# Kernel tuning notes

Measured on AMD Instinct MI355X. Metric: run time of the kernel, lower is better.

The kernel has to match this reference:

```python
import jax, jax.numpy as jnp
import numpy as np

JITTER = 1e-6
ND = 20       # num_draws
STEPS = 10    # num_steps
G = 100       # num_gammas: PG truncation terms
NUM_CLASSES = 2


def _rbf(X, outputscale, lengthscale):
    x2 = jnp.sum(X * X, axis=-1)
    d2 = jnp.maximum(x2[:, None] + x2[None, :] - 2.0 * (X @ X.T), 0.0)
    return outputscale * jnp.exp(-0.5 * d2 / (lengthscale * lengthscale))


def _chol(K):
    return jnp.linalg.cholesky(K + JITTER * jnp.eye(K.shape[-1], dtype=K.dtype))


def _pg_draw(key, c):
    # PG(1, c) via truncated infinite gamma convolution (G terms):
    # omega = (1/(2 pi^2)) * sum_k Exp(1) / ((k-1/2)^2 + c^2/(4 pi^2))
    ks = jnp.arange(1, G + 1, dtype=c.dtype)
    denom = (ks - 0.5) ** 2 + (c[..., None] ** 2) / (4.0 * jnp.pi ** 2)
    e = jax.random.exponential(key, c.shape + (G,), dtype=c.dtype)
    return jnp.sum(e / denom, axis=-1) / (2.0 * jnp.pi ** 2)


def reference(X, Y, outputscale, lengthscale):
    N = X.shape[0]
    os_ = outputscale[0]
    ls = lengthscale[0]
    K = _rbf(X, os_, ls)                          # [N,N]
    Kinv = jnp.linalg.inv(K + JITTER * jnp.eye(N, dtype=X.dtype))
    L = _chol(K)
    mu = jnp.zeros((N,), X.dtype)                 # zero mean GP
    Kinv_mu = Kinv @ mu
    y_oh = 1.0 - jax.nn.one_hot(Y, NUM_CLASSES, dtype=X.dtype)
    kappa = y_oh[:, 0] - 0.5                      # binary => 1 stick, N_sb = 1

    key = jax.random.key(42)
    k_init, k_om0, k_loop = jax.random.split(key, 3)

    # initial Gibbs state: f ~ N(mu, K) per draw
    eps0 = jax.random.normal(k_init, (ND, N), X.dtype)
    f = mu[None, :] + jnp.einsum('ij,dj->di', L, eps0)
    omega = jax.lax.stop_gradient(_pg_draw(k_om0, jax.lax.stop_gradient(f)))

    def body(state, kk):
        omega_c, f_c = state
        k1, k2 = jax.random.split(kk)
        A = Kinv[None] + jax.vmap(jnp.diag)(omega_c)         # [ND,N,N]
        sigma = jnp.linalg.inv(A)
        mu_t = jnp.einsum('dij,j->di', sigma, kappa + Kinv_mu)
        Lt = _chol(sigma)
        eps = jax.random.normal(k1, (ND, N), X.dtype)
        f_new = mu_t + jnp.einsum('dij,dj->di', Lt, eps)
        omega_new = jax.lax.stop_gradient(_pg_draw(k2, jax.lax.stop_gradient(f_new)))
        return (omega_new, f_new), None

    (omega, f), _ = jax.lax.scan(body, (omega, f), jax.random.split(k_loop, STEPS))

    # marginal log likelihood given omega (PG draws are constants)
    om = jnp.clip(omega, 1e-16)                  # [ND,N]
    Sigma_z = K[None] + jax.vmap(jnp.diag)(1.0 / om)
    Lz = _chol(Sigma_z)
    z = kappa[None, :] / om
    diff = z - mu[None, :]
    sol = jax.scipy.linalg.solve_triangular(Lz, diff[..., None], lower=True)[..., 0]
    quad = jnp.sum(sol * sol, axis=-1)
    logdet = jnp.sum(jnp.log(jnp.diagonal(Lz, axis1=-2, axis2=-1)), axis=-1)
    log2pi = float(np.log(2.0 * np.pi))
    logp = -0.5 * quad - logdet - 0.5 * N * log2pi
    mll = (logp + 0.5 * N * log2pi
           - 0.5 * jnp.sum(jnp.log(om), axis=-1)
           + 0.5 * jnp.sum(kappa[None, :] ** 2 / om, axis=-1)
           - N * float(np.log(2.0)))
    nmll = -jnp.mean(mll)
    return nmll / N


def setup_inputs() -> dict:
    key = jax.random.key(0)
    kx, ky, ko, kl = jax.random.split(key, 4)
    X = jax.random.normal(kx, (1024, 64), jnp.float32)
    Y = jax.random.randint(ky, (1024,), 0, 2)
    outputscale = jax.random.uniform(ko, (1,), jnp.float32) + 0.5
    # rescale lengthscale to ~sqrt(d) so exp(-d2/2ls^2) doesn't underflow
    lengthscale = (jax.random.uniform(kl, (1,), jnp.float32) + 0.5) * 8.0
    return {"X": X, "Y": Y, "outputscale": outputscale, "lengthscale": lengthscale}
```

## Files before the change

### kernel.cpp

```cpp
#include <hip/hip_runtime.h>
#include <stdint.h>

#define NPTS 1024
#define NDRAWS 20
#define NSTEPS 10
#define NG 100
#define PARTITIONABLE 1

#define TRI(i) (((i) * ((i) + 1)) / 2)
#define NTILE 16
#define NTRI 136
#define AST ((size_t)NTRI * 4096)

typedef unsigned int u32;

__host__ __device__ static inline void tf2x32(u32 k0, u32 k1, u32 x0, u32 x1, u32* o0, u32* o1){
  u32 ks2 = k0 ^ k1 ^ 0x1BD11BDAu;
  x0 += k0; x1 += k1;
#define TFR(r) { x0 += x1; x1 = (x1 << r) | (x1 >> (32 - r)); x1 ^= x0; }
  TFR(13) TFR(15) TFR(26) TFR(6)
  x0 += k1; x1 += ks2 + 1u;
  TFR(17) TFR(29) TFR(16) TFR(24)
  x0 += ks2; x1 += k0 + 2u;
  TFR(13) TFR(15) TFR(26) TFR(6)
  x0 += k0; x1 += k1 + 3u;
  TFR(17) TFR(29) TFR(16) TFR(24)
  x0 += k1; x1 += ks2 + 4u;
  TFR(13) TFR(15) TFR(26) TFR(6)
  x0 += ks2; x1 += k0 + 5u;
#undef TFR
  *o0 = x0; *o1 = x1;
}

__device__ static inline u32 rand32(u32 ka, u32 kb, u32 i, u32 total){
  u32 a, b;
#if PARTITIONABLE
  (void)total;
  tf2x32(ka, kb, 0u, i, &a, &b);
  return a ^ b;
#else
  u32 h = total >> 1;
  if (i < h){ tf2x32(ka, kb, i, i + h, &a, &b); return a; }
  else      { tf2x32(ka, kb, i - h, i, &a, &b); return b; }
#endif
}

__device__ static inline float u01f(u32 bits){
  return __uint_as_float(0x3F800000u | (bits >> 9)) - 1.0f;
}

__device__ static inline float erfinv32(float x){
  float w = -log1pf(-x * x);
  float p;
  if (w < 5.0f){
    w -= 2.5f;
    p = 2.81022636e-08f;
    p = fmaf(p, w, 3.43273939e-07f);
    p = fmaf(p, w, -3.5233877e-06f);
    p = fmaf(p, w, -4.39150654e-06f);
    p = fmaf(p, w, 0.00021858087f);
    p = fmaf(p, w, -0.00125372503f);
    p = fmaf(p, w, -0.00417768164f);
    p = fmaf(p, w, 0.246640727f);
    p = fmaf(p, w, 1.50140941f);
  } else {
    w = sqrtf(w) - 3.0f;
    p = -0.000200214257f;
    p = fmaf(p, w, 0.000100950558f);
    p = fmaf(p, w, 0.00134934322f);
    p = fmaf(p, w, -0.00367342844f);
    p = fmaf(p, w, 0.00573950773f);
    p = fmaf(p, w, -0.0076224613f);
    p = fmaf(p, w, 0.00943887047f);
    p = fmaf(p, w, 1.00167406f);
    p = fmaf(p, w, 2.83297682f);
  }
  return p * x;
}

__device__ static inline float normal_from_bits(u32 bits){
  const float LO = -0.99999994f;
  float u = u01f(bits);
  float v = u * 2.0f + LO;
  v = fmaxf(LO, v);
  return 1.4142135623730951f * erfinv32(v);
}

__device__ inline float  tsqrt(float x){ return sqrtf(x); }
__device__ inline double tsqrt(double x){ return sqrt(x); }
__device__ inline float  tmax(float a, float b){ return fmaxf(a, b); }
__device__ inline double tmax(double a, double b){ return fmax(a, b); }

__device__ inline void tri_decode(int p, int& ti, int& tj){
  int t = (int)((sqrtf(8.0f * (float)p + 1.0f) - 1.0f) * 0.5f);
  while ((t + 1) * (t + 2) / 2 <= p) ++t;
  while (t * (t + 1) / 2 > p) --t;
  ti = t; tj = p - t * (t + 1) / 2;
}

__device__ inline void chol_inv_64(float (*t)[65], float (*Xs)[65], float* diagL, int tid){
  for (int idx = tid; idx < 4096; idx += 256){
    int r = idx >> 6, c = idx & 63;
    Xs[r][c] = (r == c) ? 1.0f : 0.0f;
  }
  __syncthreads();
  for (int j = 0; j < 64; ++j){
    float piv = sqrtf(fmaxf(t[j][j], 1e-30f));
    float inv = 1.0f / piv;
    if (tid < 64){
      int r = j + 1 + tid;
      if (r < 64) t[r][j] *= inv;
      if (tid == 0) diagL[j] = piv;
    } else if (tid < 128){
      Xs[j][tid - 64] *= inv;
    }
    __syncthreads();
    int tg = tid >> 6, tr = tid & 63;
    for (int r2 = j + 1 + tg; r2 < 64; r2 += 4){
      float lj = t[r2][j];
      int c = j + 1 + tr;
      if (c <= r2) t[r2][c] -= lj * t[c][j];
      Xs[r2][tr] = fmaf(-lj, Xs[j][tr], Xs[r2][tr]);
    }
    __syncthreads();
  }
  if (tid < 64) t[tid][tid] = diagL[tid];
  __syncthreads();
}

__global__ __launch_bounds__(256) void k_prep(const float* X, const int* Y, float* x2, float* kappaf){
  int n = blockIdx.x * 256 + threadIdx.x;
  if (n >= NPTS) return;
  float s = 0.f;
  for (int d = 0; d < 64; ++d){ float v = X[n * 64 + d]; s += v * v; }
  x2[n] = s;
  kappaf[NPTS - 1 - n] = (float)Y[n] - 0.5f;
}

__global__ void k_computeK(const float* X, const float* x2, const float* osp, const float* lsp,
                           double* Ld){
  int j = blockIdx.x * 16 + threadIdx.x;
  int i = blockIdx.y * 16 + threadIdx.y;
  float os = osp[0], ls = lsp[0];
  float dot = 0.f;
  for (int d = 0; d < 64; ++d) dot += X[i * 64 + d] * X[j * 64 + d];
  float d2 = x2[i] + x2[j] - 2.0f * dot;
  d2 = fmaxf(d2, 0.0f);
  float kv = os * expf((-0.5f * d2) / (ls * ls));
  Ld[(size_t)i * NPTS + j] = (double)kv + (i == j ? 1e-6 : 0.0);
}

__global__ __launch_bounds__(256) void k_castL(const double* Ld, float* Lf){
  int idx = blockIdx.x * 256 + threadIdx.x;
  int i = idx >> 10, j = idx & 1023;
  Lf[idx] = (j <= i) ? (float)Ld[idx] : 0.0f;
}

__global__ __launch_bounds__(256) void k_logdetK(const double* Ld, float* ldetK){
  __shared__ double red[4];
  int tid = threadIdx.x;
  double s = 0.0;
  for (int i = tid; i < NPTS; i += 256) s += log(Ld[(size_t)i * NPTS + i]);
  for (int o = 32; o; o >>= 1) s += __shfl_down(s, o);
  if ((tid & 63) == 0) red[tid >> 6] = s;
  __syncthreads();
  if (tid == 0) ldetK[0] = (float)(2.0 * (red[0] + red[1] + red[2] + red[3]));
}

__global__ __launch_bounds__(256) void k_chol_diag_inv_d(double* M, double* Dinv, int p){
  double* DI = Dinv + (size_t)p * 4096;
  int k0 = p * 64;
  __shared__ double t[64][65];
  __shared__ double Xs[64][65];
  int tid = threadIdx.x;
  for (int idx = tid; idx < 4096; idx += 256){
    int r = idx >> 6, c = idx & 63;
    t[r][c] = (c <= r) ? M[(size_t)(k0 + r) * NPTS + k0 + c] : 0.0;
    Xs[r][c] = (r == c) ? 1.0 : 0.0;
  }
  __syncthreads();
  for (int j = 0; j < 64; ++j){
    double piv = tsqrt(tmax(t[j][j], 1e-300));
    double inv = 1.0 / piv;
    __syncthreads();
    if (tid == 0) t[j][j] = piv;
    for (int r = j + 1 + tid; r < 64; r += 256) t[r][j] *= inv;
    __syncthreads();
    int tr = tid & 63, tg = tid >> 6;
    for (int r = j + 1 + tg; r < 64; r += 4){
      int c = j + 1 + tr;
      if (c <= r) t[r][c] -= t[r][j] * t[c][j];
    }
    __syncthreads();
  }
  for (int idx = tid; idx < 4096; idx += 256){
    int r = idx >> 6, c = idx & 63;
    M[(size_t)(k0 + r) * NPTS + k0 + c] = (c <= r) ? t[r][c] : 0.0;
  }
  if (tid < 64){
    int c = tid;
    Xs[c][c] = 1.0 / t[c][c];
    for (int r = c + 1; r < 64; ++r){
      double s = 0.0;
      for (int k = c; k < r; ++k) s += t[r][k] * Xs[k][c];
      Xs[r][c] = -s / t[r][r];
    }
    for (int r = 0; r < c; ++r) Xs[r][c] = 0.0;
  }
  __syncthreads();
  for (int idx = tid; idx < 4096; idx += 256){
    int r = idx >> 6, c = idx & 63;
    DI[idx] = Xs[r][c];
  }
}

__global__ __launch_bounds__(256) void k_chol_panel_d(double* M, const double* Dinv, int p){
  const double* DI = Dinv + (size_t)p * 4096;
  int r0 = (p + 1) * 64 + blockIdx.x * 64;
  __shared__ double Rs[64][65];
  __shared__ double Ds[64][65];
  int tid = threadIdx.x;
  for (int idx = tid; idx < 4096; idx += 256){
    int r = idx >> 6, c = idx & 63;
    Rs[r][c] = M[(size_t)(r0 + r) * NPTS + p * 64 + c];
    Ds[r][c] = DI[idx];
  }
  __syncthreads();
  int tx = tid & 15, ty = tid >> 4;
  double acc[4][4];
#pragma unroll
  for (int a = 0; a < 4; ++a)
#pragma unroll
    for (int b = 0; b < 4; ++b) acc[a][b] = 0.0;
  for (int k = 0; k < 64; ++k){
    double av[4], bv[4];
#pragma unroll
    for (int a = 0; a < 4; ++a) av[a] = Rs[ty * 4 + a][k];
#pragma unroll
    for (int b = 0; b < 4; ++b) bv[b] = Ds[tx * 4 + b][k];
#pragma unroll
    for (int a = 0; a < 4; ++a)
#pragma unroll
      for (int b = 0; b < 4; ++b) acc[a][b] += av[a] * bv[b];
  }
#pragma unroll
  for (int a = 0; a < 4; ++a)
#pragma unroll
    for (int b = 0; b < 4; ++b)
      M[(size_t)(r0 + ty * 4 + a) * NPTS + p * 64 + tx * 4 + b] = acc[a][b];
}

__global__ __launch_bounds__(256) void k_chol_update_d(double* M, int k0){
  __shared__ double Pa[64][65];
  __shared__ double Pb[64][65];
  int ti, tj; tri_decode(blockIdx.x, ti, tj);
  int bi = k0 + 64 + ti * 64;
  int bj = k0 + 64 + tj * 64;
  int tid = threadIdx.x;
  for (int idx = tid; idx < 4096; idx += 256){
    int r = idx >> 6, c = idx & 63;
    Pa[r][c] = M[(size_t)(bi + r) * NPTS + k0 + c];
    Pb[r][c] = M[(size_t)(bj + r) * NPTS + k0 + c];
  }
  __syncthreads();
  int tx = tid & 15, ty = tid >> 4;
  double acc[4][4];
#pragma unroll
  for (int a = 0; a < 4; ++a)
#pragma unroll
    for (int b = 0; b < 4; ++b) acc[a][b] = 0.0;
  for (int k = 0; k < 64; ++k){
    double av[4], bv[4];
#pragma unroll
    for (int a = 0; a < 4; ++a) av[a] = Pa[ty * 4 + a][k];
#pragma unroll
    for (int b = 0; b < 4; ++b) bv[b] = Pb[tx * 4 + b][k];
#pragma unroll
    for (int a = 0; a < 4; ++a)
#pragma unroll
      for (int b = 0; b < 4; ++b) acc[a][b] += av[a] * bv[b];
  }
#pragma unroll
  for (int a = 0; a < 4; ++a)
#pragma unroll
    for (int b = 0; b < 4; ++b){
      int gi = bi + ty * 4 + a, gj = bj + tx * 4 + b;
      M[(size_t)gi * NPTS + gj] -= acc[a][b];
    }
}

static void run_chol_d(double* A, double* Dinv, hipStream_t s){
  for (int p = 0; p < 16; ++p){
    k_chol_diag_inv_d<<<dim3(1), 256, 0, s>>>(A, Dinv, p);
    int nrb = 15 - p;
    if (nrb > 0){
      k_chol_panel_d<<<dim3(nrb), 256, 0, s>>>(A, Dinv, p);
      k_chol_update_d<<<dim3(nrb * (nrb + 1) / 2), 256, 0, s>>>(A, p * 64);
    }
  }
}

__global__ __launch_bounds__(256) void k_trinv_copy_diag(const double* DinvD, double* Td){
  int p = blockIdx.x;
  for (int idx = threadIdx.x; idx < 4096; idx += 256){
    int r = idx >> 6, c = idx & 63;
    Td[(size_t)(p * 64 + r) * NPTS + p * 64 + c] = DinvD[(size_t)p * 4096 + idx];
  }
}

__global__ __launch_bounds__(256) void k_trinv_off_d(const double* Lm, double* Li, int lev){
  const double* M = Lm;
  double* O = Li;
  int J = blockIdx.x, I = J + lev;
  __shared__ double Ta[64][65];
  __shared__ double Tb[64][65];
  int tid = threadIdx.x, tx = tid & 15, ty = tid >> 4;
  double acc[4][4];
#pragma unroll
  for (int a = 0; a < 4; ++a)
#pragma unroll
    for (int b = 0; b < 4; ++b) acc[a][b] = 0.0;
  for (int K = J; K < I; ++K){
    __syncthreads();
    for (int idx = tid; idx < 4096; idx += 256){
      int r = idx >> 6, c = idx & 63;
      Ta[r][c] = M[(size_t)(I * 64 + r) * NPTS + K * 64 + c];
      Tb[r][c] = O[(size_t)(K * 64 + r) * NPTS + J * 64 + c];
    }
    __syncthreads();
    for (int k = 0; k < 64; ++k){
      double av[4], bv[4];
#pragma unroll
      for (int a = 0; a < 4; ++a) av[a] = Ta[ty * 4 + a][k];
#pragma unroll
      for (int b = 0; b < 4; ++b) bv[b] = Tb[k][tx * 4 + b];
#pragma unroll
      for (int a = 0; a < 4; ++a)
#pragma unroll
        for (int b = 0; b < 4; ++b) acc[a][b] += av[a] * bv[b];
    }
  }
  __syncthreads();
#pragma unroll
  for (int a = 0; a < 4; ++a)
#pragma unroll
    for (int b = 0; b < 4; ++b) Tb[ty * 4 + a][tx * 4 + b] = acc[a][b];
  for (int idx = tid; idx < 4096; idx += 256){
    int r = idx >> 6, c = idx & 63;
    Ta[r][c] = O[(size_t)(I * 64 + r) * NPTS + I * 64 + c];
  }
  __syncthreads();
  double ac2[4][4];
#pragma unroll
  for (int a = 0; a < 4; ++a)
#pragma unroll
    for (int b = 0; b < 4; ++b) ac2[a][b] = 0.0;
  for (int k = 0; k < 64; ++k){
    double av[4], bv[4];
#pragma unroll
    for (int a = 0; a < 4; ++a) av[a] = Ta[ty * 4 + a][k];
#pragma unroll
    for (int b = 0; b < 4; ++b) bv[b] = Tb[k][tx * 4 + b];
#pragma unroll
    for (int a = 0; a < 4; ++a)
#pragma unroll
      for (int b = 0; b < 4; ++b) ac2[a][b] += av[a] * bv[b];
  }
#pragma unroll
  for (int a = 0; a < 4; ++a)
#pragma unroll
    for (int b = 0; b < 4; ++b)
      O[(size_t)(I * 64 + ty * 4 + a) * NPTS + J * 64 + tx * 4 + b] = -ac2[a][b];
}

__global__ __launch_bounds__(256) void k_syrk_kinv_flip(const double* Td, float* Kinvp){
  int a0, b0; tri_decode(blockIdx.x, a0, b0);
  int ti = b0, tj = a0;
  int kmin = tj;
  __shared__ double Ta[64][65];
  __shared__ double Tb[64][65];
  int tid = threadIdx.x, tx = tid & 15, ty = tid >> 4;
  double acc[4][4];
#pragma unroll
  for (int a = 0; a < 4; ++a)
#pragma unroll
    for (int b = 0; b < 4; ++b) acc[a][b] = 0.0;
  for (int K = kmin; K < 16; ++K){
    __syncthreads();
    for (int idx = tid; idx < 4096; idx += 256){
      int r = idx >> 6, c = idx & 63;
      Ta[r][c] = Td[(size_t)(K * 64 + r) * NPTS + ti * 64 + c];
      Tb[r][c] = Td[(size_t)(K * 64 + r) * NPTS + tj * 64 + c];
    }
    __syncthreads();
    for (int k = 0; k < 64; ++k){
      double av[4], bv[4];
#pragma unroll
      for (int a = 0; a < 4; ++a) av[a] = Ta[k][ty * 4 + a];
#pragma unroll
      for (int b = 0; b < 4; ++b) bv[b] = Tb[k][tx * 4 + b];
#pragma unroll
      for (int a = 0; a < 4; ++a)
#pragma unroll
        for (int b = 0; b < 4; ++b) acc[a][b] += av[a] * bv[b];
    }
  }
  int tileR = 15 - ti, tileC = 15 - tj;
  float* out = Kinvp + (size_t)(TRI(tileR) + tileC) * 4096;
#pragma unroll
  for (int a = 0; a < 4; ++a)
#pragma unroll
    for (int b = 0; b < 4; ++b){
      int rin = 63 - (ty * 4 + a), cin = 63 - (tx * 4 + b);
      out[rin * 64 + cin] = (float)acc[a][b];
    }
}

__global__ __launch_bounds__(256) void k_buildA(const float* Kinvp, const float* omega, float* Ab,
                                                int c0, int clip){
  int d = c0 + blockIdx.y;
  float* A = Ab + (size_t)blockIdx.y * AST;
  int idx4 = blockIdx.x * 256 + threadIdx.x;
  float4 v = ((const float4*)Kinvp)[idx4];
  int tile = idx4 >> 10;
  int ti, tj; tri_decode(tile, ti, tj);
  if (ti == tj){
    int e = (idx4 & 1023) * 4;
    int r = e >> 6, c = e & 63;
    if (c <= r && r < c + 4){
      float om = omega[(size_t)d * NPTS + (NPTS - 1 - (ti * 64 + r))];
      if (clip) om = fmaxf(om, 1e-16f);
      ((float*)&v)[r - c] += om;
    }
  }
  ((float4*)A)[idx4] = v;
}

__global__ __launch_bounds__(256) void k_diag0(float* Ab, float* Dinv){
  float* M = Ab + (size_t)blockIdx.x * AST;
  float* DI = Dinv + (size_t)blockIdx.x * 16 * 4096;
  __shared__ float t[64][65];
  __shared__ float Xs[64][65];
  __shared__ float diagL[64];
  int tid = threadIdx.x;
  for (int idx = tid; idx < 1024; idx += 256){
    float4 v = ((const float4*)M)[idx];
    int e = idx * 4, r = e >> 6, c = e & 63;
    t[r][c] = v.x; t[r][c + 1] = v.y; t[r][c + 2] = v.z; t[r][c + 3] = v.w;
  }
  __syncthreads();
  chol_inv_64(t, Xs, diagL, tid);
  for (int idx = tid; idx < 1024; idx += 256){
    int e = idx * 4, r = e >> 6, c = e & 63;
    float4 v, w;
    v.x = (c     <= r) ? t[r][c]     : 0.f;
    v.y = (c + 1 <= r) ? t[r][c + 1] : 0.f;
    v.z = (c + 2 <= r) ? t[r][c + 2] : 0.f;
    v.w = (c + 3 <= r) ? t[r][c + 3] : 0.f;
    w.x = Xs[r][c]; w.y = Xs[r][c + 1]; w.z = Xs[r][c + 2]; w.w = Xs[r][c + 3];
    ((float4*)M)[idx] = v;
    ((float4*)DI)[idx] = w;
  }
}

__global__ __launch_bounds__(256) void k_panel(float* Ab, const float* Dinv, int p){
  float* M = Ab + (size_t)blockIdx.y * AST;
  const float* DI = Dinv + ((size_t)blockIdx.y * 16 + p) * 4096;
  int rt = p + 1 + blockIdx.x;
  float* R = M + (size_t)(TRI(rt) + p) * 4096;
  __shared__ float Rs[64][65];
  __shared__ float Ds[64][65];
  int tid = threadIdx.x;
  for (int idx = tid; idx < 1024; idx += 256){
    float4 v = ((const float4*)R)[idx];
    float4 w = ((const float4*)DI)[idx];
    int e = idx * 4, r = e >> 6, c = e & 63;
    Rs[r][c] = v.x; Rs[r][c + 1] = v.y; Rs[r][c + 2] = v.z; Rs[r][c + 3] = v.w;
    Ds[r][c] = w.x; Ds[r][c + 1] = w.y; Ds[r][c + 2] = w.z; Ds[r][c + 3] = w.w;
  }
  __syncthreads();
  int tx = tid & 15, ty = tid >> 4;
  float acc[4][4];
#pragma unroll
  for (int a = 0; a < 4; ++a)
#pragma unroll
    for (int b = 0; b < 4; ++b) acc[a][b] = 0.f;
  for (int k = 0; k < 64; ++k){
    float av[4], bv[4];
#pragma unroll
    for (int a = 0; a < 4; ++a) av[a] = Rs[ty * 4 + a][k];
#pragma unroll
    for (int b = 0; b < 4; ++b) bv[b] = Ds[tx * 4 + b][k];
#pragma unroll
    for (int a = 0; a < 4; ++a)
#pragma unroll
      for (int b = 0; b < 4; ++b) acc[a][b] += av[a] * bv[b];
  }
  __syncthreads();
#pragma unroll
  for (int a = 0; a < 4; ++a)
#pragma unroll
    for (int b = 0; b < 4; ++b) Rs[ty * 4 + a][tx * 4 + b] = acc[a][b];
  __syncthreads();
  for (int idx = tid; idx < 1024; idx += 256){
    int e = idx * 4, r = e >> 6, c = e & 63;
    float4 v;
    v.x = Rs[r][c]; v.y = Rs[r][c + 1]; v.z = Rs[r][c + 2]; v.w = Rs[r][c + 3];
    ((float4*)R)[idx] = v;
  }
}

__global__ __launch_bounds__(256) void k_update_diag(float* Ab, float* Dinv, int p){
  float* M = Ab + (size_t)blockIdx.y * AST;
  __shared__ float Pa[64][65];
  __shared__ float Pb[64][65];
  __shared__ float diagL[64];
  int t0, t1; tri_decode(blockIdx.x, t0, t1);
  int bi = p + 1 + t0, bj = p + 1 + t1;
  const float* La = M + (size_t)(TRI(bi) + p) * 4096;
  const float* Lb = M + (size_t)(TRI(bj) + p) * 4096;
  float* Atile = M + (size_t)(TRI(bi) + bj) * 4096;
  int tid = threadIdx.x;
  for (int idx = tid; idx < 1024; idx += 256){
    float4 v = ((const float4*)La)[idx];
    float4 w = ((const float4*)Lb)[idx];
    int e = idx * 4, r = e >> 6, c = e & 63;
    Pa[r][c] = v.x; Pa[r][c + 1] = v.y; Pa[r][c + 2] = v.z; Pa[r][c + 3] = v.w;
    Pb[r][c] = w.x; Pb[r][c + 1] = w.y; Pb[r][c + 2] = w.z; Pb[r][c + 3] = w.w;
  }
  __syncthreads();
  int tx = tid & 15, ty = tid >> 4;
  float acc[4][4];
#pragma unroll
  for (int a = 0; a < 4; ++a)
#pragma unroll
    for (int b = 0; b < 4; ++b) acc[a][b] = 0.f;
  for (int k = 0; k < 64; ++k){
    float av[4], bv[4];
#pragma unroll
    for (int a = 0; a < 4; ++a) av[a] = Pa[ty * 4 + a][k];
#pragma unroll
    for (int b = 0; b < 4; ++b) bv[b] = Pb[tx * 4 + b][k];
#pragma unroll
    for (int a = 0; a < 4; ++a)
#pragma unroll
      for (int b = 0; b < 4; ++b) acc[a][b] += av[a] * bv[b];
  }
  __syncthreads();
  for (int idx = tid; idx < 1024; idx += 256){
    float4 v = ((const float4*)Atile)[idx];
    int e = idx * 4, r = e >> 6, c = e & 63;
    Pa[r][c] = v.x; Pa[r][c + 1] = v.y; Pa[r][c + 2] = v.z; Pa[r][c + 3] = v.w;
  }
  __syncthreads();
#pragma unroll
  for (int a = 0; a < 4; ++a)
#pragma unroll
    for (int b = 0; b < 4; ++b)
      Pa[ty * 4 + a][tx * 4 + b] -= acc[a][b];
  __syncthreads();
  if (blockIdx.x == 0){
    float* DI = Dinv + ((size_t)blockIdx.y * 16 + (p + 1)) * 4096;
    chol_inv_64(Pa, Pb, diagL, tid);
    for (int idx = tid; idx < 1024; idx += 256){
      int e = idx * 4, r = e >> 6, c = e & 63;
      float4 v, w;
      v.x = (c     <= r) ? Pa[r][c]     : 0.f;
      v.y = (c + 1 <= r) ? Pa[r][c + 1] : 0.f;
      v.z = (c + 2 <= r) ? Pa[r][c + 2] : 0.f;
      v.w = (c + 3 <= r) ? Pa[r][c + 3] : 0.f;
      w.x = Pb[r][c]; w.y = Pb[r][c + 1]; w.z = Pb[r][c + 2]; w.w = Pb[r][c + 3];
      ((float4*)Atile)[idx] = v;
      ((float4*)DI)[idx] = w;
    }
  } else {
    for (int idx = tid; idx < 1024; idx += 256){
      int e = idx * 4, r = e >> 6, c = e & 63;
      float4 v;
      v.x = Pa[r][c]; v.y = Pa[r][c + 1]; v.z = Pa[r][c + 2]; v.w = Pa[r][c + 3];
      ((float4*)Atile)[idx] = v;
    }
  }
}

static void run_chol_f(float* A, float* Dinv, int batch, hipStream_t s){
  k_diag0<<<dim3(batch), 256, 0, s>>>(A, Dinv);
  for (int p = 0; p < 15; ++p){
    int nrb = 15 - p;
    k_panel<<<dim3(nrb, batch), 256, 0, s>>>(A, Dinv, p);
    k_update_diag<<<dim3(nrb * (nrb + 1) / 2, batch), 256, 0, s>>>(A, Dinv, p);
  }
}

__global__ __launch_bounds__(256) void k_fwd_solve(const float* Ab, const float* DinvF,
                                                   const float* kappaf, float* zbuf){
  int d0 = blockIdx.x;
  const float* L = Ab + (size_t)d0 * AST;
  const float* DI = DinvF + (size_t)d0 * 16 * 4096;
  __shared__ float z[NPTS];
  __shared__ float buf[2][64 * 65];
  __shared__ float part[4][64];
  int tid = threadIdx.x;
  float4 rg[4];
  auto loadDI = [&](int p){
#pragma unroll
    for (int j = 0; j < 4; ++j)
      rg[j] = *(const float4*)&DI[p * 4096 + j * 1024 + tid * 4];
  };
  auto loadL = [&](int rbrow, int pcol){
    const float* T = L + (size_t)(TRI(rbrow) + pcol) * 4096;
#pragma unroll
    for (int j = 0; j < 4; ++j)
      rg[j] = *(const float4*)&T[j * 1024 + tid * 4];
  };
  auto store = [&](int cur){
#pragma unroll
    for (int j = 0; j < 4; ++j){
      int e = j * 1024 + tid * 4; int r = e >> 6, c = e & 63;
      float* b = &buf[cur][r * 65 + c];
      b[0] = rg[j].x; b[1] = rg[j].y; b[2] = rg[j].z; b[3] = rg[j].w;
    }
  };
  for (int i = tid; i < NPTS; i += 256) z[i] = kappaf[i];
  loadDI(0);
  int cur = 0;
  for (int p = 0; p < 16; ++p){
    for (int rb = p; rb < 16; ++rb){
      store(cur);
      int np = p, nrb = rb + 1;
      if (nrb >= 16){ np = p + 1; nrb = np; }
      if (np < 16){ if (nrb == np) loadDI(np); else loadL(nrb, np); }
      __syncthreads();
      int rr = tid & 63, q = tid >> 6;
      float s = 0.f;
#pragma unroll
      for (int cc = 0; cc < 16; ++cc)
        s += buf[cur][rr * 65 + q * 16 + cc] * z[p * 64 + q * 16 + cc];
      part[q][rr] = s;
      __syncthreads();
      if (tid < 64){
        float v = part[0][tid] + part[1][tid] + part[2][tid] + part[3][tid];
        if (rb == p) z[p * 64 + tid] = v;
        else z[rb * 64 + tid] -= v;
      }
      __syncthreads();
      cur ^= 1;
    }
  }
  for (int i = tid; i < NPTS; i += 256) zbuf[(size_t)d0 * NPTS + i] = z[i];
}

__global__ __launch_bounds__(256) void k_back_solve_f(const float* Ab, const float* DinvF,
                                                      const float* zbuf, const float* eps,
                                                      float* fbuf, int c0){
  int d0 = blockIdx.x, d = c0 + d0;
  const float* L = Ab + (size_t)d0 * AST;
  const float* DI = DinvF + (size_t)d0 * 16 * 4096;
  __shared__ float z1[NPTS], z2[NPTS];
  __shared__ float buf[2][64 * 65];
  __shared__ float p1[4][64], p2[4][64];
  int tid = threadIdx.x;
  float4 rg[4];
  auto loadDI = [&](int p){
#pragma unroll
    for (int j = 0; j < 4; ++j)
      rg[j] = *(const float4*)&DI[p * 4096 + j * 1024 + tid * 4];
  };
  auto loadL = [&](int prow, int cbcol){
    const float* T = L + (size_t)(TRI(prow) + cbcol) * 4096;
#pragma unroll
    for (int j = 0; j < 4; ++j)
      rg[j] = *(const float4*)&T[j * 1024 + tid * 4];
  };
  auto store = [&](int cur){
#pragma unroll
    for (int j = 0; j < 4; ++j){
      int e = j * 1024 + tid * 4; int r = e >> 6, c = e & 63;
      float* b = &buf[cur][r * 65 + c];
      b[0] = rg[j].x; b[1] = rg[j].y; b[2] = rg[j].z; b[3] = rg[j].w;
    }
  };
  for (int i = tid; i < NPTS; i += 256){
    z1[i] = zbuf[(size_t)d0 * NPTS + i];
    z2[NPTS - 1 - i] = eps[(size_t)d * NPTS + i];
  }
  loadDI(15);
  int cur = 0;
  for (int p = 15; p >= 0; --p){
    for (int cb = p; cb >= 0; --cb){
      store(cur);
      int np = p, ncb = cb - 1;
      if (ncb < 0){ np = p - 1; ncb = np; }
      if (np >= 0){ if (ncb == np) loadDI(np); else loadL(np, ncb); }
      __syncthreads();
      int cc = tid & 63, q = tid >> 6;
      float s1 = 0.f, s2 = 0.f;
#pragma unroll
      for (int rr = 0; rr < 16; ++rr){
        float t = buf[cur][(q * 16 + rr) * 65 + cc];
        s1 += t * z1[p * 64 + q * 16 + rr];
        s2 += t * z2[p * 64 + q * 16 + rr];
      }
      p1[q][cc] = s1; p2[q][cc] = s2;
      __syncthreads();
      if (tid < 64){
        float v1 = p1[0][tid] + p1[1][tid] + p1[2][tid] + p1[3][tid];
        float v2 = p2[0][tid] + p2[1][tid] + p2[2][tid] + p2[3][tid];
        if (cb == p){ z1[p * 64 + tid] = v1; z2[p * 64 + tid] = v2; }
        else { z1[cb * 64 + tid] -= v1; z2[cb * 64 + tid] -= v2; }
      }
      __syncthreads();
      cur ^= 1;
    }
  }
  for (int i = tid; i < NPTS; i += 256)
    fbuf[(size_t)d * NPTS + i] = z1[NPTS - 1 - i] + z2[NPTS - 1 - i];
}

__global__ __launch_bounds__(256) void k_final3(const float* Ab, const float* DinvF,
                                                const float* kappaf, const float* ldetK,
                                                float* mll, int c0){
  int d0 = blockIdx.x, d = c0 + d0;
  const float* L = Ab + (size_t)d0 * AST;
  const float* DI = DinvF + (size_t)d0 * 16 * 4096;
  __shared__ float z[NPTS];
  __shared__ float buf[2][64 * 65];
  __shared__ float part[4][64];
  __shared__ float redq[4];
  int tid = threadIdx.x;
  float4 rg[4];
  auto loadDI = [&](int p){
#pragma unroll
    for (int j = 0; j < 4; ++j)
      rg[j] = *(const float4*)&DI[p * 4096 + j * 1024 + tid * 4];
  };
  auto loadL = [&](int rbrow, int pcol){
    const float* T = L + (size_t)(TRI(rbrow) + pcol) * 4096;
#pragma unroll
    for (int j = 0; j < 4; ++j)
      rg[j] = *(const float4*)&T[j * 1024 + tid * 4];
  };
  auto store = [&](int cur){
#pragma unroll
    for (int j = 0; j < 4; ++j){
      int e = j * 1024 + tid * 4; int r = e >> 6, c = e & 63;
      float* b = &buf[cur][r * 65 + c];
      b[0] = rg[j].x; b[1] = rg[j].y; b[2] = rg[j].z; b[3] = rg[j].w;
    }
  };
  for (int i = tid; i < NPTS; i += 256) z[i] = kappaf[i];
  loadDI(0);
  int cur = 0;
  float ldacc = 0.f;
  for (int p = 0; p < 16; ++p){
    for (int rb = p; rb < 16; ++rb){
      store(cur);
      int np = p, nrb = rb + 1;
      if (nrb >= 16){ np = p + 1; nrb = np; }
      if (np < 16){ if (nrb == np) loadDI(np); else loadL(nrb, np); }
      __syncthreads();
      if (rb == p && tid < 64) ldacc += logf(buf[cur][tid * 65 + tid]);
      int rr = tid & 63, q = tid >> 6;
      float s = 0.f;
#pragma unroll
      for (int cc = 0; cc < 16; ++cc)
        s += buf[cur][rr * 65 + q * 16 + cc] * z[p * 64 + q * 16 + cc];
      part[q][rr] = s;
      __syncthreads();
      if (tid < 64){
        float v = part[0][tid] + part[1][tid] + part[2][tid] + part[3][tid];
// ... 43 lines not shown
      float4 v = *(const float4*)&Lf[(size_t)(rb * 64 + rr) * NPTS + kt * 64 + cc];
      tile[rr][cc] = v.x; tile[rr][cc + 1] = v.y; tile[rr][cc + 2] = v.z; tile[rr][cc + 3] = v.w;
    }
    if (tid < 64) ev[tid] = eps[(size_t)d * NPTS + kt * 64 + tid];
    __syncthreads();
    int cmax = (kt == rb) ? (r + 1) : 64;
    for (int cc = q * 16; cc < q * 16 + 16; ++cc){
      if (cc < cmax) acc += tile[r][cc] * ev[cc];
    }
  }
  part[q][r] = acc;
  __syncthreads();
  if (tid < 64){
    float s = part[0][tid] + part[1][tid] + part[2][tid] + part[3][tid];
    f[(size_t)d * NPTS + rb * 64 + tid] = s;
  }
}

__global__ __launch_bounds__(256) void k_pg(u32 ka, u32 kb, const float* f, float* omega){
  int idx = blockIdx.x * 256 + threadIdx.x;
  if (idx >= NDRAWS * NPTS) return;
  float c = f[idx];
  float c2w = (c * c) / 39.47841760435743f;
  float sum = 0.f;
  u32 base = (u32)idx * NG;
  for (int g = 0; g < NG; ++g){
    u32 bits = rand32(ka, kb, base + (u32)g, (u32)(NDRAWS * NPTS * NG));
    float u = u01f(bits);
    float e = -log1pf(-u);
    float kk = (float)g + 0.5f;
    sum += e / (kk * kk + c2w);
  }
  omega[idx] = sum / 19.739208802178716f;
}

__global__ void k_out(const float* mll, float* out){
  if (threadIdx.x == 0){
    float s = 0.f;
    for (int dd = 0; dd < NDRAWS; ++dd) s += mll[dd];
    float m = s / (float)NDRAWS;
    out[0] = (-m) / (float)NPTS;
  }
}

static void host_split(u32 ka, u32 kb, int num, u32* outA, u32* outB){
#if PARTITIONABLE
  for (int j = 0; j < num; ++j) tf2x32(ka, kb, 0u, (u32)j, &outA[j], &outB[j]);
#else
  u32 flat[40];
  for (int k = 0; k < num; ++k){
    u32 a, b; tf2x32(ka, kb, (u32)k, (u32)(num + k), &a, &b);
    flat[k] = a; flat[num + k] = b;
  }
  for (int j = 0; j < num; ++j){ outA[j] = flat[2 * j]; outB[j] = flat[2 * j + 1]; }
#endif
}

extern "C" void kernel_launch(void* const* d_in, const int* in_sizes, int n_in,
                              void* d_out, int out_size, void* d_ws, size_t ws_size,
                              hipStream_t stream){
  const float* X  = (const float*)d_in[0];
  const int*   Y  = (const int*)d_in[1];
  const float* osp = (const float*)d_in[2];
  const float* lsp = (const float*)d_in[3];
  float* out = (float*)d_out;

  const size_t NN = (size_t)NPTS * NPTS;
  char* p = (char*)d_ws;
  float* Kinvp  = (float*)p;  p += AST * 4;
  float* omega  = (float*)p;  p += (size_t)NDRAWS * NPTS * 4;
  float* fbuf   = (float*)p;  p += (size_t)NDRAWS * NPTS * 4;
  float* epsb   = (float*)p;  p += (size_t)NDRAWS * NPTS * 4;
  float* kappaf = (float*)p;  p += NPTS * 4;
  float* x2     = (float*)p;  p += NPTS * 4;
  float* mll    = (float*)p;  p += 128;
  float* ldetK  = (float*)p;  p += 128;
  uintptr_t ip = (uintptr_t)p; ip = (ip + 255) & ~(uintptr_t)255;
  char* cb = (char*)ip;

  double* Ld    = (double*)cb;
  double* Td    = (double*)(cb + NN * 8);
  double* DinvD = (double*)(cb + NN * 16);
  float*  Lf    = (float*)(cb + NN * 16 + (size_t)16 * 4096 * 8);

  size_t rem = ws_size - (size_t)(cb - (char*)d_ws);
  const size_t PER_DRAW = AST * 4 + (size_t)16 * 4096 * 4 + NPTS * 4;
  int CH = (int)(rem / PER_DRAW);
  if (CH > NDRAWS) CH = NDRAWS;
  if (CH < 1) CH = 1;
  float* bufA  = (float*)cb;
  float* dinvF = (float*)(cb + (size_t)CH * AST * 4);
  float* zbuf  = (float*)(cb + (size_t)CH * (AST * 4 + (size_t)16 * 4096 * 4));

  u32 r3A[3], r3B[3];
  host_split(0u, 42u, 3, r3A, r3B);
  u32 kiA = r3A[0], kiB = r3B[0];
  u32 koA = r3A[1], koB = r3B[1];
  u32 klA = r3A[2], klB = r3B[2];
  u32 kkA[NSTEPS], kkB[NSTEPS];
  host_split(klA, klB, NSTEPS, kkA, kkB);
  u32 k1A[NSTEPS], k1B[NSTEPS], k2A[NSTEPS], k2B[NSTEPS];
  for (int t = 0; t < NSTEPS; ++t){
    u32 sA[2], sB[2];
    host_split(kkA[t], kkB[t], 2, sA, sB);
    k1A[t] = sA[0]; k1B[t] = sB[0];
    k2A[t] = sA[1]; k2B[t] = sB[1];
  }

  k_prep<<<dim3(4), 256, 0, stream>>>(X, Y, x2, kappaf);
  k_computeK<<<dim3(64, 64), dim3(16, 16), 0, stream>>>(X, x2, osp, lsp, Ld);
  run_chol_d(Ld, DinvD, stream);
  k_castL<<<dim3(4096), 256, 0, stream>>>(Ld, Lf);
  k_logdetK<<<dim3(1), 256, 0, stream>>>(Ld, ldetK);
  k_trinv_copy_diag<<<dim3(16), 256, 0, stream>>>(DinvD, Td);
  for (int lev = 1; lev < 16; ++lev)
    k_trinv_off_d<<<dim3(16 - lev), 256, 0, stream>>>(Ld, Td, lev);
  k_syrk_kinv_flip<<<dim3(NTRI), 256, 0, stream>>>(Td, Kinvp);

  k_gen_eps<<<dim3(80), 256, 0, stream>>>(kiA, kiB, epsb);
  k_init_f2<<<dim3(16, NDRAWS), 256, 0, stream>>>(Lf, epsb, fbuf);
  k_pg<<<dim3(80), 256, 0, stream>>>(koA, koB, fbuf, omega);

  for (int t = 0; t < NSTEPS; ++t){
    k_gen_eps<<<dim3(80), 256, 0, stream>>>(k1A[t], k1B[t], epsb);
    for (int c0 = 0; c0 < NDRAWS; c0 += CH){
      int nb = NDRAWS - c0 < CH ? NDRAWS - c0 : CH;
      k_buildA<<<dim3(544, nb), 256, 0, stream>>>(Kinvp, omega, bufA, c0, 0);
      run_chol_f(bufA, dinvF, nb, stream);
      k_fwd_solve<<<dim3(nb), 256, 0, stream>>>(bufA, dinvF, kappaf, zbuf);
      k_back_solve_f<<<dim3(nb), 256, 0, stream>>>(bufA, dinvF, zbuf, epsb, fbuf, c0);
    }
    k_pg<<<dim3(80), 256, 0, stream>>>(k2A[t], k2B[t], fbuf, omega);
  }

  for (int c0 = 0; c0 < NDRAWS; c0 += CH){
    int nb = NDRAWS - c0 < CH ? NDRAWS - c0 : CH;
    k_buildA<<<dim3(544, nb), 256, 0, stream>>>(Kinvp, omega, bufA, c0, 1);
    run_chol_f(bufA, dinvF, nb, stream);
    k_final3<<<dim3(nb), 256, 0, stream>>>(bufA, dinvF, kappaf, ldetK, mll, c0);
  }
  k_out<<<dim3(1), 64, 0, stream>>>(mll, out);
}
```

Baseline: 24.89 ms.

## Transpose GEMM tiles, split triangular inverse into parallel parts, fuse solves

Several changes land together. The float Cholesky panel and update kernels now stage tiles transposed with a padded stride, so inner-loop operands are read as float4 and results go straight to global memory without an extra shared-memory pass. Off-diagonal update blocks subtract in registers, and only the diagonal block runs the factor and inverse. The double triangular inverse splits each level into a parallel partial-product kernel plus a reduction kernel, and the double diagonal factor reuses a shared templated Cholesky-with-inverse routine. The forward and backward solves fuse into one kernel, which removes a global round trip through zbuf but adds scratch space and extra launches for the inverse.

New measurement: 23.16 ms. 1.07x faster.

```diff
diff --git a/kernel.cpp b/kernel.cpp
--- a/kernel.cpp
+++ b/kernel.cpp
@@ -8,7 +8,6 @@
 #define PARTITIONABLE 1
 
 #define TRI(i) (((i) * ((i) + 1)) / 2)
-#define NTILE 16
 #define NTRI 136
 #define AST ((size_t)NTRI * 4096)
 
@@ -98,33 +97,34 @@
   ti = t; tj = p - t * (t + 1) / 2;
 }
 
-__device__ inline void chol_inv_64(float (*t)[65], float (*Xs)[65], float* diagL, int tid){
+template<typename T, int S>
+__device__ inline void chol_inv_64t(T* t, T* Xs, T* diagL, int tid){
   for (int idx = tid; idx < 4096; idx += 256){
     int r = idx >> 6, c = idx & 63;
-    Xs[r][c] = (r == c) ? 1.0f : 0.0f;
+    Xs[r * S + c] = (r == c) ? (T)1 : (T)0;
   }
   __syncthreads();
   for (int j = 0; j < 64; ++j){
-    float piv = sqrtf(fmaxf(t[j][j], 1e-30f));
-    float inv = 1.0f / piv;
+    T piv = tsqrt(tmax(t[j * S + j], (T)1e-30));
+    T inv = (T)1 / piv;
     if (tid < 64){
       int r = j + 1 + tid;
-      if (r < 64) t[r][j] *= inv;
+      if (r < 64) t[r * S + j] *= inv;
       if (tid == 0) diagL[j] = piv;
     } else if (tid < 128){
-      Xs[j][tid - 64] *= inv;
+      Xs[j * S + (tid - 64)] *= inv;
     }
     __syncthreads();
     int tg = tid >> 6, tr = tid & 63;
     for (int r2 = j + 1 + tg; r2 < 64; r2 += 4){
-      float lj = t[r2][j];
+      T lj = t[r2 * S + j];
       int c = j + 1 + tr;
-      if (c <= r2) t[r2][c] -= lj * t[c][j];
-      Xs[r2][tr] = fmaf(-lj, Xs[j][tr], Xs[r2][tr]);
+      if (c <= r2) t[r2 * S + c] -= lj * t[c * S + j];
+      Xs[r2 * S + tr] = Xs[r2 * S + tr] - lj * Xs[j * S + tr];
     }
     __syncthreads();
   }
-  if (tid < 64) t[tid][tid] = diagL[tid];
+  if (tid < 64) t[tid * S + tid] = diagL[tid];
   __syncthreads();
 }
 
@@ -172,44 +172,17 @@
   int k0 = p * 64;
   __shared__ double t[64][65];
   __shared__ double Xs[64][65];
+  __shared__ double diagL[64];
   int tid = threadIdx.x;
   for (int idx = tid; idx < 4096; idx += 256){
     int r = idx >> 6, c = idx & 63;
     t[r][c] = (c <= r) ? M[(size_t)(k0 + r) * NPTS + k0 + c] : 0.0;
-    Xs[r][c] = (r == c) ? 1.0 : 0.0;
-  }
-  __syncthreads();
-  for (int j = 0; j < 64; ++j){
-    double piv = tsqrt(tmax(t[j][j], 1e-300));
-    double inv = 1.0 / piv;
-    __syncthreads();
-    if (tid == 0) t[j][j] = piv;
-    for (int r = j + 1 + tid; r < 64; r += 256) t[r][j] *= inv;
-    __syncthreads();
-    int tr = tid & 63, tg = tid >> 6;
-    for (int r = j + 1 + tg; r < 64; r += 4){
-      int c = j + 1 + tr;
-      if (c <= r) t[r][c] -= t[r][j] * t[c][j];
-    }
-    __syncthreads();
-  }
+  }
+  __syncthreads();
+  chol_inv_64t<double, 65>(&t[0][0], &Xs[0][0], &diagL[0], tid);
   for (int idx = tid; idx < 4096; idx += 256){
     int r = idx >> 6, c = idx & 63;
     M[(size_t)(k0 + r) * NPTS + k0 + c] = (c <= r) ? t[r][c] : 0.0;
-  }
-  if (tid < 64){
-    int c = tid;
-    Xs[c][c] = 1.0 / t[c][c];
-    for (int r = c + 1; r < 64; ++r){
-      double s = 0.0;
-      for (int k = c; k < r; ++k) s += t[r][k] * Xs[k][c];
-      Xs[r][c] = -s / t[r][r];
-    }
-    for (int r = 0; r < c; ++r) Xs[r][c] = 0.0;
-  }
-  __syncthreads();
-  for (int idx = tid; idx < 4096; idx += 256){
-    int r = idx >> 6, c = idx & 63;
     DI[idx] = Xs[r][c];
   }
 }
@@ -308,46 +281,54 @@
   }
 }
 
-__global__ __launch_bounds__(256) void k_trinv_off_d(const double* Lm, double* Li, int lev){
-  const double* M = Lm;
-  double* O = Li;
+__global__ __launch_bounds__(256) void k_trinv_part(const double* Lm, const double* Td,
+                                                    double* Gs, int lev){
+  int J = blockIdx.x, s = blockIdx.y;
+  int I = J + lev, K = J + s;
+  __shared__ double Ta[64][65];
+  __shared__ double Tb[64][65];
+  int tid = threadIdx.x, tx = tid & 15, ty = tid >> 4;
+  for (int idx = tid; idx < 4096; idx += 256){
+    int r = idx >> 6, c = idx & 63;
+    Ta[r][c] = Lm[(size_t)(I * 64 + r) * NPTS + K * 64 + c];
+    Tb[r][c] = Td[(size_t)(K * 64 + r) * NPTS + J * 64 + c];
+  }
+  __syncthreads();
+  double acc[4][4];
+#pragma unroll
+  for (int a = 0; a < 4; ++a)
+#pragma unroll
+    for (int b = 0; b < 4; ++b) acc[a][b] = 0.0;
+  for (int k = 0; k < 64; ++k){
+    double av[4], bv[4];
+#pragma unroll
+    for (int a = 0; a < 4; ++a) av[a] = Ta[ty * 4 + a][k];
+#pragma unroll
+    for (int b = 0; b < 4; ++b) bv[b] = Tb[k][tx * 4 + b];
+#pragma unroll
+    for (int a = 0; a < 4; ++a)
+#pragma unroll
+      for (int b = 0; b < 4; ++b) acc[a][b] += av[a] * bv[b];
+  }
+  double* out = Gs + ((size_t)J * 15 + s) * 4096;
+#pragma unroll
+  for (int a = 0; a < 4; ++a)
+#pragma unroll
+    for (int b = 0; b < 4; ++b)
+      out[(ty * 4 + a) * 64 + tx * 4 + b] = acc[a][b];
+}
+
+__global__ __launch_bounds__(256) void k_trinv_fin(double* Td, const double* Gs, int lev){
   int J = blockIdx.x, I = J + lev;
   __shared__ double Ta[64][65];
   __shared__ double Tb[64][65];
   int tid = threadIdx.x, tx = tid & 15, ty = tid >> 4;
-  double acc[4][4];
-#pragma unroll
-  for (int a = 0; a < 4; ++a)
-#pragma unroll
-    for (int b = 0; b < 4; ++b) acc[a][b] = 0.0;
-  for (int K = J; K < I; ++K){
-    __syncthreads();
-    for (int idx = tid; idx < 4096; idx += 256){
-      int r = idx >> 6, c = idx & 63;
-      Ta[r][c] = M[(size_t)(I * 64 + r) * NPTS + K * 64 + c];
-      Tb[r][c] = O[(size_t)(K * 64 + r) * NPTS + J * 64 + c];
-    }
-    __syncthreads();
-    for (int k = 0; k < 64; ++k){
-      double av[4], bv[4];
-#pragma unroll
-      for (int a = 0; a < 4; ++a) av[a] = Ta[ty * 4 + a][k];
-#pragma unroll
-      for (int b = 0; b < 4; ++b) bv[b] = Tb[k][tx * 4 + b];
-#pragma unroll
-      for (int a = 0; a < 4; ++a)
-#pragma unroll
-        for (int b = 0; b < 4; ++b) acc[a][b] += av[a] * bv[b];
-    }
-  }
-  __syncthreads();
-#pragma unroll
-  for (int a = 0; a < 4; ++a)
-#pragma unroll
-    for (int b = 0; b < 4; ++b) Tb[ty * 4 + a][tx * 4 + b] = acc[a][b];
   for (int idx = tid; idx < 4096; idx += 256){
     int r = idx >> 6, c = idx & 63;
-    Ta[r][c] = O[(size_t)(I * 64 + r) * NPTS + I * 64 + c];
+    double g = 0.0;
+    for (int s = 0; s < lev; ++s) g += Gs[((size_t)J * 15 + s) * 4096 + idx];
+    Tb[r][c] = g;
+    Ta[r][c] = Td[(size_t)(I * 64 + r) * NPTS + I * 64 + c];
   }
   __syncthreads();
   double ac2[4][4];
@@ -370,7 +351,7 @@
   for (int a = 0; a < 4; ++a)
 #pragma unroll
     for (int b = 0; b < 4; ++b)
-      O[(size_t)(I * 64 + ty * 4 + a) * NPTS + J * 64 + tx * 4 + b] = -ac2[a][b];
+      Td[(size_t)(I * 64 + ty * 4 + a) * NPTS + J * 64 + tx * 4 + b] = -ac2[a][b];
 }
 
 __global__ __launch_bounds__(256) void k_syrk_kinv_flip(const double* Td, float* Kinvp){
@@ -449,7 +430,7 @@
     t[r][c] = v.x; t[r][c + 1] = v.y; t[r][c + 2] = v.z; t[r][c + 3] = v.w;
   }
   __syncthreads();
-  chol_inv_64(t, Xs, diagL, tid);
+  chol_inv_64t<float, 65>(&t[0][0], &Xs[0][0], &diagL[0], tid);
   for (int idx = tid; idx < 1024; idx += 256){
     int e = idx * 4, r = e >> 6, c = e & 63;
     float4 v, w;
@@ -468,15 +449,17 @@
   const float* DI = Dinv + ((size_t)blockIdx.y * 16 + p) * 4096;
   int rt = p + 1 + blockIdx.x;
   float* R = M + (size_t)(TRI(rt) + p) * 4096;
-  __shared__ float Rs[64][65];
-  __shared__ float Ds[64][65];
+  __shared__ __align__(16) float Rst[64 * 68];
+  __shared__ __align__(16) float Dst[64 * 68];
   int tid = threadIdx.x;
   for (int idx = tid; idx < 1024; idx += 256){
     float4 v = ((const float4*)R)[idx];
     float4 w = ((const float4*)DI)[idx];
     int e = idx * 4, r = e >> 6, c = e & 63;
-    Rs[r][c] = v.x; Rs[r][c + 1] = v.y; Rs[r][c + 2] = v.z; Rs[r][c + 3] = v.w;
-    Ds[r][c] = w.x; Ds[r][c + 1] = w.y; Ds[r][c + 2] = w.z; Ds[r][c + 3] = w.w;
+    Rst[(c + 0) * 68 + r] = v.x; Rst[(c + 1) * 68 + r] = v.y;
+    Rst[(c + 2) * 68 + r] = v.z; Rst[(c + 3) * 68 + r] = v.w;
+    Dst[(c + 0) * 68 + r] = w.x; Dst[(c + 1) * 68 + r] = w.y;
+    Dst[(c + 2) * 68 + r] = w.z; Dst[(c + 3) * 68 + r] = w.w;
   }
   __syncthreads();
   int tx = tid & 15, ty = tid >> 4;
@@ -486,34 +469,27 @@
 #pragma unroll
     for (int b = 0; b < 4; ++b) acc[a][b] = 0.f;
   for (int k = 0; k < 64; ++k){
-    float av[4], bv[4];
-#pragma unroll
-    for (int a = 0; a < 4; ++a) av[a] = Rs[ty * 4 + a][k];
-#pragma unroll
-    for (int b = 0; b < 4; ++b) bv[b] = Ds[tx * 4 + b][k];
+    float4 av4 = *(const float4*)&Rst[k * 68 + ty * 4];
+    float4 bv4 = *(const float4*)&Dst[k * 68 + tx * 4];
+    float av[4] = {av4.x, av4.y, av4.z, av4.w};
+    float bv[4] = {bv4.x, bv4.y, bv4.z, bv4.w};
 #pragma unroll
     for (int a = 0; a < 4; ++a)
 #pragma unroll
       for (int b = 0; b < 4; ++b) acc[a][b] += av[a] * bv[b];
   }
-  __syncthreads();
-#pragma unroll
-  for (int a = 0; a < 4; ++a)
-#pragma unroll
-    for (int b = 0; b < 4; ++b) Rs[ty * 4 + a][tx * 4 + b] = acc[a][b];
-  __syncthreads();
-  for (int idx = tid; idx < 1024; idx += 256){
-    int e = idx * 4, r = e >> 6, c = e & 63;
+#pragma unroll
+  for (int a = 0; a < 4; ++a){
     float4 v;
-    v.x = Rs[r][c]; v.y = Rs[r][c + 1]; v.z = Rs[r][c + 2]; v.w = Rs[r][c + 3];
-    ((float4*)R)[idx] = v;
+    v.x = acc[a][0]; v.y = acc[a][1]; v.z = acc[a][2]; v.w = acc[a][3];
+    *((float4*)&R[(size_t)(ty * 4 + a) * 64 + tx * 4]) = v;
   }
 }
 
 __global__ __launch_bounds__(256) void k_update_diag(float* Ab, float* Dinv, int p){
   float* M = Ab + (size_t)blockIdx.y * AST;
-  __shared__ float Pa[64][65];
-  __shared__ float Pb[64][65];
+  __shared__ __align__(16) float Pat[64 * 68];
+  __shared__ __align__(16) float Pbt[64 * 68];
   __shared__ float diagL[64];
   int t0, t1; tri_decode(blockIdx.x, t0, t1);
   int bi = p + 1 + t0, bj = p + 1 + t1;
@@ -525,8 +501,10 @@
     float4 v = ((const float4*)La)[idx];
     float4 w = ((const float4*)Lb)[idx];
     int e = idx * 4, r = e >> 6, c = e & 63;
-    Pa[r][c] = v.x; Pa[r][c + 1] = v.y; Pa[r][c + 2] = v.z; Pa[r][c + 3] = v.w;
-    Pb[r][c] = w.x; Pb[r][c + 1] = w.y; Pb[r][c + 2] = w.z; Pb[r][c + 3] = w.w;
+    Pat[(c + 0) * 68 + r] = v.x; Pat[(c + 1) * 68 + r] = v.y;
+    Pat[(c + 2) * 68 + r] = v.z; Pat[(c + 3) * 68 + r] = v.w;
+    Pbt[(c + 0) * 68 + r] = w.x; Pbt[(c + 1) * 68 + r] = w.y;
+    Pbt[(c + 2) * 68 + r] = w.z; Pbt[(c + 3) * 68 + r] = w.w;
   }
   __syncthreads();
   int tx = tid & 15, ty = tid >> 4;
@@ -536,49 +514,50 @@
 #pragma unroll
     for (int b = 0; b < 4; ++b) acc[a][b] = 0.f;
   for (int k = 0; k < 64; ++k){
-    float av[4], bv[4];
-#pragma unroll
-    for (int a = 0; a < 4; ++a) av[a] = Pa[ty * 4 + a][k];
-#pragma unroll
-    for (int b = 0; b < 4; ++b) bv[b] = Pb[tx * 4 + b][k];
+    float4 av4 = *(const float4*)&Pat[k * 68 + ty * 4];
+    float4 bv4 = *(const float4*)&Pbt[k * 68 + tx * 4];
+    float av[4] = {av4.x, av4.y, av4.z, av4.w};
+    float bv[4] = {bv4.x, bv4.y, bv4.z, bv4.w};
 #pragma unroll
     for (int a = 0; a < 4; ++a)
 #pragma unroll
       for (int b = 0; b < 4; ++b) acc[a][b] += av[a] * bv[b];
   }
-  __syncthreads();
-  for (int idx = tid; idx < 1024; idx += 256){
-    float4 v = ((const float4*)Atile)[idx];
-    int e = idx * 4, r = e >> 6, c = e & 63;
-    Pa[r][c] = v.x; Pa[r][c + 1] = v.y; Pa[r][c + 2] = v.z; Pa[r][c + 3] = v.w;
-  }
-  __syncthreads();
-#pragma unroll
-  for (int a = 0; a < 4; ++a)
-#pragma unroll
-    for (int b = 0; b < 4; ++b)
-      Pa[ty * 4 + a][tx * 4 + b] -= acc[a][b];
-  __syncthreads();
   if (blockIdx.x == 0){
+    __syncthreads();
+    for (int idx = tid; idx < 1024; idx += 256){
+      float4 v = ((const float4*)Atile)[idx];
+      int e = idx * 4, r = e >> 6, c = e & 63;
+      Pat[r * 68 + c] = v.x; Pat[r * 68 + c + 1] = v.y;
+      Pat[r * 68 + c + 2] = v.z; Pat[r * 68 + c + 3] = v.w;
+    }
+    __syncthreads();
+#pragma unroll
+    for (int a = 0; a < 4; ++a)
+#pragma unroll
+      for (int b = 0; b < 4; ++b)
+        Pat[(ty * 4 + a) * 68 + tx * 4 + b] -= acc[a][b];
+    __syncthreads();
+    chol_inv_64t<float, 68>(Pat, Pbt, &diagL[0], tid);
     float* DI = Dinv + ((size_t)blockIdx.y * 16 + (p + 1)) * 4096;
-    chol_inv_64(Pa, Pb, diagL, tid);
     for (int idx = tid; idx < 1024; idx += 256){
       int e = idx * 4, r = e >> 6, c = e & 63;
       float4 v, w;
-      v.x = (c     <= r) ? Pa[r][c]     : 0.f;
-      v.y = (c + 1 <= r) ? Pa[r][c + 1] : 0.f;
-      v.z = (c + 2 <= r) ? Pa[r][c + 2] : 0.f;
-      v.w = (c + 3 <= r) ? Pa[r][c + 3] : 0.f;
-      w.x = Pb[r][c]; w.y = Pb[r][c + 1]; w.z = Pb[r][c + 2]; w.w = Pb[r][c + 3];
+      v.x = (c     <= r) ? Pat[r * 68 + c]     : 0.f;
+      v.y = (c + 1 <= r) ? Pat[r * 68 + c + 1] : 0.f;
+      v.z = (c + 2 <= r) ? Pat[r * 68 + c + 2] : 0.f;
+      v.w = (c + 3 <= r) ? Pat[r * 68 + c + 3] : 0.f;
+      w.x = Pbt[r * 68 + c]; w.y = Pbt[r * 68 + c + 1];
+      w.z = Pbt[r * 68 + c + 2]; w.w = Pbt[r * 68 + c + 3];
       ((float4*)Atile)[idx] = v;
       ((float4*)DI)[idx] = w;
     }
   } else {
-    for (int idx = tid; idx < 1024; idx += 256){
-      int e = idx * 4, r = e >> 6, c = e & 63;
-      float4 v;
-      v.x = Pa[r][c]; v.y = Pa[r][c + 1]; v.z = Pa[r][c + 2]; v.w = Pa[r][c + 3];
-      ((float4*)Atile)[idx] = v;
+#pragma unroll
+    for (int a = 0; a < 4; ++a){
+      float4 v = *((const float4*)&Atile[(size_t)(ty * 4 + a) * 64 + tx * 4]);
+      v.x -= acc[a][0]; v.y -= acc[a][1]; v.z -= acc[a][2]; v.w -= acc[a][3];
+      *((float4*)&Atile[(size_t)(ty * 4 + a) * 64 + tx * 4]) = v;
     }
   }
 }
@@ -592,14 +571,15 @@
   }
 }
 
-__global__ __launch_bounds__(256) void k_fwd_solve(const float* Ab, const float* DinvF,
-                                                   const float* kappaf, float* zbuf){
-  int d0 = blockIdx.x;
+__global__ __launch_bounds__(256) void k_step_solve(const float* Ab, const float* DinvF,
+                                                    const float* kappaf, const float* eps,
+                                                    float* fbuf, int c0){
+  int d0 = blockIdx.x, d = c0 + d0;
   const float* L = Ab + (size_t)d0 * AST;
   const float* DI = DinvF + (size_t)d0 * 16 * 4096;
-  __shared__ float z[NPTS];
+  __shared__ float z1[NPTS], z2[NPTS];
   __shared__ float buf[2][64 * 65];
-  __shared__ float part[4][64];
+  __shared__ float p1[4][64], p2[4][64];
   int tid = threadIdx.x;
   float4 rg[4];
   auto loadDI = [&](int p){
@@ -607,8 +587,8 @@
     for (int j = 0; j < 4; ++j)
       rg[j] = *(const float4*)&DI[p * 4096 + j * 1024 + tid * 4];
   };
-  auto loadL = [&](int rbrow, int pcol){
-    const float* T = L + (size_t)(TRI(rbrow) + pcol) * 4096;
+  auto loadL = [&](int row, int col){
+    const float* T = L + (size_t)(TRI(row) + col) * 4096;
 #pragma unroll
     for (int j = 0; j < 4; ++j)
       rg[j] = *(const float4*)&T[j * 1024 + tid * 4];
@@ -621,7 +601,10 @@
       b[0] = rg[j].x; b[1] = rg[j].y; b[2] = rg[j].z; b[3] = rg[j].w;
     }
   };
-  for (int i = tid; i < NPTS; i += 256) z[i] = kappaf[i];
+  for (int i = tid; i < NPTS; i += 256){
+    z1[i] = kappaf[i];
+    z2[NPTS - 1 - i] = eps[(size_t)d * NPTS + i];
+  }
   loadDI(0);
   int cur = 0;
   for (int p = 0; p < 16; ++p){
@@ -635,57 +618,19 @@
       float s = 0.f;
 #pragma unroll
       for (int cc = 0; cc < 16; ++cc)
-        s += buf[cur][rr * 65 + q * 16 + cc] * z[p * 64 + q * 16 + cc];
-      part[q][rr] = s;
+        s += buf[cur][rr * 65 + q * 16 + cc] * z1[p * 64 + q * 16 + cc];
+      p1[q][rr] = s;
       __syncthreads();
       if (tid < 64){
-        float v = part[0][tid] + part[1][tid] + part[2][tid] + part[3][tid];
-        if (rb == p) z[p * 64 + tid] = v;
-        else z[rb * 64 + tid] -= v;
+        float v = p1[0][tid] + p1[1][tid] + p1[2][tid] + p1[3][tid];
+        if (rb == p) z1[p * 64 + tid] = v;
+        else z1[rb * 64 + tid] -= v;
       }
       __syncthreads();
       cur ^= 1;
     }
   }
-  for (int i = tid; i < NPTS; i += 256) zbuf[(size_t)d0 * NPTS + i] = z[i];
-}
-
-__global__ __launch_bounds__(256) void k_back_solve_f(const float* Ab, const float* DinvF,
-                                                      const float* zbuf, const float* eps,
-                                                      float* fbuf, int c0){
-  int d0 = blockIdx.x, d = c0 + d0;
-  const float* L = Ab + (size_t)d0 * AST;
-  const float* DI = DinvF + (size_t)d0 * 16 * 4096;
-  __shared__ float z1[NPTS], z2[NPTS];
-  __shared__ float buf[2][64 * 65];
-  __shared__ float p1[4][64], p2[4][64];
-  int tid = threadIdx.x;
-  float4 rg[4];
-  auto loadDI = [&](int p){
-#pragma unroll
-    for (int j = 0; j < 4; ++j)
-      rg[j] = *(const float4*)&DI[p * 4096 + j * 1024 + tid * 4];
-  };
-  auto loadL = [&](int prow, int cbcol){
-    const float* T = L + (size_t)(TRI(prow) + cbcol) * 4096;
-#pragma unroll
-    for (int j = 0; j < 4; ++j)
-      rg[j] = *(const float4*)&T[j * 1024 + tid * 4];
-  };
-  auto store = [&](int cur){
-#pragma unroll
-    for (int j = 0; j < 4; ++j){
-      int e = j * 1024 + tid * 4; int r = e >> 6, c = e & 63;
-      float* b = &buf[cur][r * 65 + c];
-      b[0] = rg[j].x; b[1] = rg[j].y; b[2] = rg[j].z; b[3] = rg[j].w;
-    }
-  };
-  for (int i = tid; i < NPTS; i += 256){
-    z1[i] = zbuf[(size_t)d0 * NPTS + i];
-    z2[NPTS - 1 - i] = eps[(size_t)d * NPTS + i];
-  }
   loadDI(15);
-  int cur = 0;
   for (int p = 15; p >= 0; --p){
     for (int cb = p; cb >= 0; --cb){
       store(cur);
@@ -895,15 +840,15 @@
   double* Td    = (double*)(cb + NN * 8);
   double* DinvD = (double*)(cb + NN * 16);
   float*  Lf    = (float*)(cb + NN * 16 + (size_t)16 * 4096 * 8);
+  double* Gslc  = (double*)(cb + NN * 16 + (size_t)16 * 4096 * 8 + NN * 4);
 
   size_t rem = ws_size - (size_t)(cb - (char*)d_ws);
-  const size_t PER_DRAW = AST * 4 + (size_t)16 * 4096 * 4 + NPTS * 4;
+  const size_t PER_DRAW = AST * 4 + (size_t)16 * 4096 * 4;
   int CH = (int)(rem / PER_DRAW);
   if (CH > NDRAWS) CH = NDRAWS;
   if (CH < 1) CH = 1;
   float* bufA  = (float*)cb;
   float* dinvF = (float*)(cb + (size_t)CH * AST * 4);
-  float* zbuf  = (float*)(cb + (size_t)CH * (AST * 4 + (size_t)16 * 4096 * 4));
 
   u32 r3A[3], r3B[3];
   host_split(0u, 42u, 3, r3A, r3B);
@@ -926,8 +871,10 @@
   k_castL<<<dim3(4096), 256, 0, stream>>>(Ld, Lf);
   k_logdetK<<<dim3(1), 256, 0, stream>>>(Ld, ldetK);
   k_trinv_copy_diag<<<dim3(16), 256, 0, stream>>>(DinvD, Td);
-  for (int lev = 1; lev < 16; ++lev)
-    k_trinv_off_d<<<dim3(16 - lev), 256, 0, stream>>>(Ld, Td, lev);
+  for (int lev = 1; lev < 16; ++lev){
+    k_trinv_part<<<dim3(16 - lev, lev), 256, 0, stream>>>(Ld, Td, Gslc, lev);
+    k_trinv_fin<<<dim3(16 - lev), 256, 0, stream>>>(Td, Gslc, lev);
+  }
   k_syrk_kinv_flip<<<dim3(NTRI), 256, 0, stream>>>(Td, Kinvp);
 
   k_gen_eps<<<dim3(80), 256, 0, stream>>>(kiA, kiB, epsb);
@@ -940,8 +887,7 @@
       int nb = NDRAWS - c0 < CH ? NDRAWS - c0 : CH;
       k_buildA<<<dim3(544, nb), 256, 0, stream>>>(Kinvp, omega, bufA, c0, 0);
       run_chol_f(bufA, dinvF, nb, stream);
-      k_fwd_solve<<<dim3(nb), 256, 0, stream>>>(bufA, dinvF, kappaf, zbuf);
-      k_back_solve_f<<<dim3(nb), 256, 0, stream>>>(bufA, dinvF, zbuf, epsb, fbuf, c0);
+      k_step_solve<<<dim3(nb), 256, 0, stream>>>(bufA, dinvF, kappaf, epsb, fbuf, c0);
     }
     k_pg<<<dim3(80), 256, 0, stream>>>(k2A[t], k2B[t], fbuf, omega);
   }
```
